# Performance work log

Measured on AMD Instinct MI355X. Metric: run time of the kernel, lower is better.

## Reference

```python
import jax, jax.numpy as jnp
import numpy as np

B, CN, T = 16, 22, 1000
EXP, FCH, SPD, NCLS = 300, 150, 100, 4
KS = (15, 75, 55)
_IU = np.triu_indices(SPD)
_VEC_SCALE = np.where(_IU[0] == _IU[1], 1.0, np.sqrt(2.0)).astype(np.float32)


def _ln(x, g, b, eps=1e-5):
    m = x.mean(-1, keepdims=True)
    v = x.var(-1, keepdims=True)
    return (x - m) / jnp.sqrt(v + eps) * g + b


def _block(x, w1, w2, w3, w4, g1, b1, w5, g2, b2):
    # x: (B, CN, T). Conv2d(1,1,(3,1), same) over electrode axis.
    h = jax.lax.conv_general_dilated(x[:, None], w1.reshape(1, 1, 3, 1), (1, 1),
                                     [(1, 1), (0, 0)],
                                     dimension_numbers=('NCHW', 'OIHW', 'NCHW'))[:, 0]
    # Conv2d(1, 300, (1,1)): pure channel broadcast-expand
    h = h[:, None, :, :] * w2[None, :, None, None]          # (B, EXP, CN, T)
    # Conv2dWithConstraint: depthwise spatial conv (groups=300) with max-norm=1 on each filter
    n = jnp.linalg.norm(w3, axis=1, keepdims=True)
    w3r = w3 * jnp.minimum(1.0, 1.0 / (n + 1e-12))
    h = jnp.einsum('bgct,gc->bgt', h, w3r)                  # height collapses -> (B, EXP, T)
    h = jnp.einsum('og,bgt->bot', w4, h)                    # pointwise -> (B, FCH, T)
    h = _ln(h, g1, b1)
    K = w5.shape[-1]
    # depthwise temporal conv, padding='same' (odd K)
    h = jax.lax.conv_general_dilated(h, w5, (1,), [(K // 2, K // 2)],
                                     dimension_numbers=('NCH', 'OIH', 'NCH'),
                                     feature_group_count=FCH)
    return _ln(h, g2, b2)


def setup_inputs():
    key = jax.random.key(0)
    ks = jax.random.split(key, 64)
    d = {'x': jax.random.normal(ks[0], (B, CN, T), jnp.float32)}
    i = 1
    for bi, K in zip((1, 2, 3), KS):
        d[f'b{bi}_w1'] = jax.random.normal(ks[i], (3,)) / np.sqrt(3); i += 1
        d[f'b{bi}_w2'] = jax.random.normal(ks[i], (EXP,)); i += 1
        d[f'b{bi}_w3'] = jax.random.normal(ks[i], (EXP, CN)) / np.sqrt(CN); i += 1
        d[f'b{bi}_w4'] = jax.random.normal(ks[i], (FCH, EXP)) / np.sqrt(EXP); i += 1
        d[f'b{bi}_g1'] = jnp.ones((T,)); d[f'b{bi}_b1'] = jnp.zeros((T,))
        d[f'b{bi}_w5'] = jax.random.normal(ks[i], (FCH, 1, K)) / np.sqrt(K); i += 1
        d[f'b{bi}_g2'] = jnp.ones((T,)); d[f'b{bi}_b2'] = jnp.zeros((T,))
    d['w_sconv'] = jax.random.normal(ks[i], (SPD, 3 * FCH)) / np.sqrt(3 * FCH); i += 1
    d['w_aff'] = jnp.eye(SPD) + 0.05 * jax.random.normal(ks[i], (SPD, SPD)); i += 1
    d['w_fc'] = jax.random.normal(ks[i], (NCLS, SPD * (SPD + 1) // 2)) / np.sqrt(SPD * (SPD + 1) // 2); i += 1
    d['b_fc'] = jnp.zeros((NCLS,))
    return d


def reference(x,
              b1_w1, b1_w2, b1_w3, b1_w4, b1_g1, b1_b1, b1_w5, b1_g2, b1_b2,
              b2_w1, b2_w2, b2_w3, b2_w4, b2_g1, b2_b1, b2_w5, b2_g2, b2_b2,
              b3_w1, b3_w2, b3_w3, b3_w4, b3_g1, b3_b1, b3_w5, b3_g2, b3_b2,
              w_sconv, w_aff, w_fc, b_fc):
    h1 = _block(x, b1_w1, b1_w2, b1_w3, b1_w4, b1_g1, b1_b1, b1_w5, b1_g2, b1_b2)
    h2 = _block(x, b2_w1, b2_w2, b2_w3, b2_w4, b2_g1, b2_b1, b2_w5, b2_g2, b2_b2)
    h3 = _block(x, b3_w1, b3_w2, b3_w3, b3_w4, b3_g1, b3_b1, b3_w5, b3_g2, b3_b2)
    h = jnp.concatenate([h1, h2, h3], axis=1)               # (B, 450, T)
    h = jnp.einsum('oi,bit->bot', w_sconv, h)               # (B, SPD, T)
    # PCOM: covariance pooling over time -> SPD matrix per sample
    xc = h - h.mean(-1, keepdims=True)
    cov = jnp.einsum('bit,bjt->bij', xc, xc) / (T - 1) + 1e-4 * jnp.eye(SPD)
    # AffineInvariantLayer: learnable congruence transform W P W^T
    P = jnp.einsum('ij,bjk,lk->bil', w_aff, cov, w_aff)
    # LogmLayer: matrix log via batched eigendecomposition
    w, v = jnp.linalg.eigh(P)
    L = jnp.einsum('bik,bk,bjk->bij', v, jnp.log(jnp.clip(w, 1e-6)), v)
    # Vec: upper-triangular half-vectorization (off-diag * sqrt(2)) -> 5050
    flat = L[:, _IU[0], _IU[1]] * _VEC_SCALE
    logits = flat @ w_fc.T + b_fc
    return (logits, flat)
```

## Files before the change

kernel.cpp:

```cpp
#include <hip/hip_runtime.h>

#define B_ 16
#define CN_ 22
#define T_ 1000
#define EXP_ 300
#define FCH_ 150
#define SPD_ 100
#define NSWEEP 8

static constexpr unsigned long long OFF_M2   = 0ull;
static constexpr unsigned long long OFF_HCAT = 65536ull;
static constexpr unsigned long long OFF_XC   = OFF_HCAT + 28800000ull;
static constexpr unsigned long long OFF_COV  = OFF_XC   + 6400000ull;
static constexpr unsigned long long OFF_T1   = OFF_COV  + 640000ull;
static constexpr unsigned long long OFF_P    = OFF_T1   + 640000ull;
static constexpr unsigned long long OFF_G    = OFF_XC;

struct PrepPtrs  { const float* w1[3]; const float* w2[3]; const float* w3[3]; const float* w4[3]; };
struct FrontPtrs { const float* g1[3]; const float* b1[3]; const float* w5[3];
                   const float* g2[3]; const float* b2[3]; int K[3]; };

__device__ __forceinline__ float block_sum(float v, float* sbuf) {
  #pragma unroll
  for (int off = 32; off > 0; off >>= 1) v += __shfl_down(v, off, 64);
  const int wid  = threadIdx.x >> 6;
  const int lane = threadIdx.x & 63;
  const int nw   = blockDim.x >> 6;
  if (lane == 0) sbuf[wid] = v;
  __syncthreads();
  float r = 0.f;
  for (int w = 0; w < nw; ++w) r += sbuf[w];
  __syncthreads();
  return r;
}

__device__ __forceinline__ float dpp_shr1(float old_, float src) {
  return __builtin_bit_cast(float, __builtin_amdgcn_update_dpp(
      __builtin_bit_cast(int, old_), __builtin_bit_cast(int, src),
      0x138, 0xf, 0xf, false));
}
__device__ __forceinline__ float dpp_shl1(float old_, float src) {
  return __builtin_bit_cast(float, __builtin_amdgcn_update_dpp(
      __builtin_bit_cast(int, old_), __builtin_bit_cast(int, src),
      0x130, 0xf, 0xf, false));
}

__global__ __launch_bounds__(256) void k_prep(PrepPtrs pp, float* __restrict__ M2) {
  const int beta = blockIdx.x;
  __shared__ float w3r[EXP_*CN_];
  __shared__ float M[FCH_*CN_];
  const float* w1 = pp.w1[beta];
  const float* w2 = pp.w2[beta];
  const float* w3 = pp.w3[beta];
  const float* w4 = pp.w4[beta];

  for (int g = threadIdx.x; g < EXP_; g += 256) {
    float s = 0.f;
    for (int c = 0; c < CN_; ++c) { float w = w3[g*CN_ + c]; s += w*w; }
    float n = sqrtf(s);
    float scale = fminf(1.f, 1.f/(n + 1e-12f)) * w2[g];
    for (int c = 0; c < CN_; ++c) w3r[g*CN_ + c] = w3[g*CN_ + c] * scale;
  }
  __syncthreads();
  for (int idx = threadIdx.x; idx < FCH_*CN_; idx += 256) {
    int o = idx / CN_, c = idx - o*CN_;
    float acc = 0.f;
    for (int g = 0; g < EXP_; ++g) acc += w4[o*EXP_ + g] * w3r[g*CN_ + c];
    M[idx] = acc;
  }
  __syncthreads();
  const float k0 = w1[0], k1 = w1[1], k2 = w1[2];
  for (int idx = threadIdx.x; idx < FCH_*CN_; idx += 256) {
    int c = idx % CN_;
    float v = k1 * M[idx];
    if (c > 0)       v += k2 * M[idx - 1];
    if (c < CN_ - 1) v += k0 * M[idx + 1];
    M2[beta*FCH_*CN_ + idx] = v;
  }
}

__global__ __launch_bounds__(256) void k_front(const float* __restrict__ x,
                                               const float* __restrict__ M2,
                                               FrontPtrs fp,
                                               float* __restrict__ hcat) {
  const int wg   = blockIdx.x;
  const int beta = wg / (B_*FCH_);
  const int rem  = wg - beta*(B_*FCH_);
  const int b    = rem / FCH_;
  const int o    = rem - b*FCH_;
  const int K    = fp.K[beta];
  const int Kh   = K >> 1;

  __shared__ float m2[CN_];
  __shared__ float hb2[T_];
  __shared__ float w5s[80];
  __shared__ float red[8];

  if (threadIdx.x < CN_) m2[threadIdx.x] = M2[(beta*FCH_ + o)*CN_ + threadIdx.x];
  if (threadIdx.x < K)   w5s[threadIdx.x] = fp.w5[beta][o*K + threadIdx.x];
  __syncthreads();

  const float* xb = x + (size_t)b*CN_*T_;
  float hv[4];
  float psum = 0.f;
  #pragma unroll
  for (int e = 0; e < 4; ++e) {
    int t = threadIdx.x + 256*e;
    float acc = 0.f;
    if (t < T_) {
      #pragma unroll
      for (int c = 0; c < CN_; ++c) acc += m2[c] * xb[c*T_ + t];
    }
    hv[e] = acc; psum += acc;
  }
  float mean = block_sum(psum, red) * (1.f/T_);
  float pv = 0.f;
  #pragma unroll
  for (int e = 0; e < 4; ++e) { int t = threadIdx.x + 256*e; if (t < T_) { float d = hv[e]-mean; pv += d*d; } }
  float var = block_sum(pv, red) * (1.f/T_);
  float inv = rsqrtf(var + 1e-5f);
  const float* g1 = fp.g1[beta]; const float* b1 = fp.b1[beta];
  #pragma unroll
  for (int e = 0; e < 4; ++e) { int t = threadIdx.x + 256*e; if (t < T_) hb2[t] = (hv[e]-mean)*inv*g1[t] + b1[t]; }
  __syncthreads();

  float cv[4];
  float ps2 = 0.f;
  #pragma unroll
  for (int e = 0; e < 4; ++e) {
    int t = threadIdx.x + 256*e;
    float acc = 0.f;
    if (t < T_) {
      int lo = t - Kh;
      for (int k = 0; k < K; ++k) {
        int tt = lo + k;
        float hvv = (tt >= 0 && tt < T_) ? hb2[tt] : 0.f;
        acc += hvv * w5s[k];
      }
    }
    cv[e] = acc; ps2 += acc;
  }
  float mean2 = block_sum(ps2, red) * (1.f/T_);
  float pv2 = 0.f;
  #pragma unroll
  for (int e = 0; e < 4; ++e) { int t = threadIdx.x + 256*e; if (t < T_) { float d = cv[e]-mean2; pv2 += d*d; } }
  float var2 = block_sum(pv2, red) * (1.f/T_);
  float inv2 = rsqrtf(var2 + 1e-5f);
  const float* g2 = fp.g2[beta]; const float* b2 = fp.b2[beta];
  float* hrow = hcat + ((size_t)b*(3*FCH_) + beta*FCH_ + o)*T_;
  #pragma unroll
  for (int e = 0; e < 4; ++e) { int t = threadIdx.x + 256*e; if (t < T_) hrow[t] = (cv[e]-mean2)*inv2*g2[t] + b2[t]; }
}

__global__ __launch_bounds__(256) void k_sconv(const float* __restrict__ hcat,
                                               const float* __restrict__ wsc,
                                               float* __restrict__ xc) {
  const int b  = blockIdx.x / 10;
  const int s0 = (blockIdx.x % 10) * 10;
  __shared__ float ws[10*450];
  __shared__ float red[8];
  for (int idx = threadIdx.x; idx < 4500; idx += 256) {
    int s = idx / 450, i = idx - s*450;
    ws[idx] = wsc[(s0+s)*450 + i];
  }
  __syncthreads();
  float acc[10][4];
  #pragma unroll
  for (int s = 0; s < 10; ++s)
    #pragma unroll
    for (int e = 0; e < 4; ++e) acc[s][e] = 0.f;
  const float* hb = hcat + (size_t)b*450*T_;
  for (int i = 0; i < 450; ++i) {
    float xv[4];
    #pragma unroll
    for (int e = 0; e < 4; ++e) { int t = threadIdx.x + 256*e; xv[e] = (t < T_) ? hb[(size_t)i*T_ + t] : 0.f; }
    #pragma unroll
    for (int s = 0; s < 10; ++s) {
      float w = ws[s*450 + i];
      #pragma unroll
      for (int e = 0; e < 4; ++e) acc[s][e] += w * xv[e];
    }
  }
  for (int s = 0; s < 10; ++s) {
    float mu = block_sum(acc[s][0]+acc[s][1]+acc[s][2]+acc[s][3], red) * (1.f/T_);
    float* xr = xc + ((size_t)b*SPD_ + s0 + s)*T_;
    #pragma unroll
    for (int e = 0; e < 4; ++e) { int t = threadIdx.x + 256*e; if (t < T_) xr[t] = acc[s][e] - mu; }
  }
}

__global__ __launch_bounds__(256) void k_cov(const float* __restrict__ xc, float* __restrict__ cov) {
  const int b  = blockIdx.x / 5;
  const int j0 = (blockIdx.x % 5) * 20;
  __shared__ __align__(16) float xst[SPD_*100];
  const int it = threadIdx.x / 10;
  const int jj = threadIdx.x - it*10;
  const bool act = threadIdx.x < 250;
  double a64[4][2] = {{0.0,0.0},{0.0,0.0},{0.0,0.0},{0.0,0.0}};
  for (int ch = 0; ch < 10; ++ch) {
    __syncthreads();
    const int tc0 = ch*100;
    for (int idx = threadIdx.x; idx < SPD_*100; idx += 256) {
      int row = idx / 100, tt = idx - row*100;
      xst[idx] = xc[((size_t)b*SPD_ + row)*T_ + tc0 + tt];
    }
    __syncthreads();
    if (act) {
      float a32[4][2] = {{0,0},{0,0},{0,0},{0,0}};
      for (int t4 = 0; t4 < 100; t4 += 4) {
        float4 xi[4], xj[2];
        #pragma unroll
        for (int r = 0; r < 4; ++r) xi[r] = *(const float4*)&xst[(it + 25*r)*100 + t4];
        #pragma unroll
        for (int s = 0; s < 2; ++s) xj[s] = *(const float4*)&xst[(j0 + jj + 10*s)*100 + t4];
        #pragma unroll
        for (int r = 0; r < 4; ++r)
          #pragma unroll
          for (int s = 0; s < 2; ++s)
            a32[r][s] += xi[r].x*xj[s].x + xi[r].y*xj[s].y + xi[r].z*xj[s].z + xi[r].w*xj[s].w;
      }
      #pragma unroll
      for (int r = 0; r < 4; ++r)
        #pragma unroll
        for (int s = 0; s < 2; ++s) a64[r][s] += (double)a32[r][s];
    }
  }
  if (act) {
    #pragma unroll
    for (int r = 0; r < 4; ++r) {
      #pragma unroll
      for (int s = 0; s < 2; ++s) {
        int i = it + 25*r, j = j0 + jj + 10*s;
        double v = a64[r][s] * (1.0/999.0);
        if (i == j) v += 1e-4;
        cov[(size_t)b*SPD_*SPD_ + i*SPD_ + j] = (float)v;
      }
    }
  }
}

__global__ __launch_bounds__(256) void k_aff1(const float* __restrict__ cov,
                                              const float* __restrict__ waff,
                                              float* __restrict__ T1) {
  const int b  = blockIdx.x / 5;
  const int j0 = (blockIdx.x % 5) * 20;
  __shared__ float Cs[SPD_*101];
  __shared__ float Ws[20*100];
  for (int idx = threadIdx.x; idx < SPD_*SPD_; idx += 256) {
    int r = idx / 100, c = idx - r*100;
    Cs[r*101 + c] = cov[(size_t)b*SPD_*SPD_ + idx];
  }
  for (int idx = threadIdx.x; idx < 2000; idx += 256) {
    int jl = idx / 100, k = idx - jl*100;
    Ws[idx] = waff[(j0+jl)*100 + k];
  }
  __syncthreads();
  if (threadIdx.x < 250) {
    const int it = threadIdx.x / 10, jj = threadIdx.x % 10;
    double acc[4][2] = {{0.0,0.0},{0.0,0.0},{0.0,0.0},{0.0,0.0}};
    for (int k = 0; k < 100; ++k) {
      double cvv[4], wv[2];
      #pragma unroll
      for (int r = 0; r < 4; ++r) cvv[r] = (double)Cs[(it + 25*r)*101 + k];
      #pragma unroll
      for (int s = 0; s < 2; ++s) wv[s] = (double)Ws[(jj + 10*s)*100 + k];
      #pragma unroll
      for (int r = 0; r < 4; ++r)
        #pragma unroll
        for (int s = 0; s < 2; ++s) acc[r][s] += cvv[r]*wv[s];
    }
    #pragma unroll
    for (int r = 0; r < 4; ++r)
      #pragma unroll
      for (int s = 0; s < 2; ++s)
        T1[(size_t)b*SPD_*SPD_ + (it + 25*r)*100 + (j0 + jj + 10*s)] = (float)acc[r][s];
  }
}

__global__ __launch_bounds__(256) void k_aff2(const float* __restrict__ T1,
                                              const float* __restrict__ waff,
                                              float* __restrict__ P) {
  const int b  = blockIdx.x / 5;
  const int j0 = (blockIdx.x % 5) * 20;
  __shared__ float T1s[100*20];
  for (int idx = threadIdx.x; idx < 2000; idx += 256) {
    int k = idx / 20, jl = idx - k*20;
    T1s[idx] = T1[(size_t)b*SPD_*SPD_ + k*100 + j0 + jl];
  }
  __syncthreads();
  if (threadIdx.x < 250) {
    const int it = threadIdx.x / 10, jj = threadIdx.x % 10;
    double acc[4][2] = {{0.0,0.0},{0.0,0.0},{0.0,0.0},{0.0,0.0}};
    for (int k = 0; k < 100; ++k) {
      double wv[4], tv[2];
      #pragma unroll
      for (int r = 0; r < 4; ++r) wv[r] = (double)waff[(it + 25*r)*100 + k];
      #pragma unroll
      for (int s = 0; s < 2; ++s) tv[s] = (double)T1s[k*20 + jj + 10*s];
      #pragma unroll
      for (int r = 0; r < 4; ++r)
        #pragma unroll
        for (int s = 0; s < 2; ++s) acc[r][s] += wv[r]*tv[s];
    }
    #pragma unroll
    for (int r = 0; r < 4; ++r)
      #pragma unroll
      for (int s = 0; s < 2; ++s)
        P[(size_t)b*SPD_*SPD_ + (it + 25*r)*100 + (j0 + jj + 10*s)] = (float)acc[r][s];
  }
}

__global__ __launch_bounds__(256)
__attribute__((amdgpu_waves_per_eu(1, 1)))
void k_eig(const float* __restrict__ P, float* __restrict__ Gout) {
  __shared__ __align__(16) float gbuf[2][256];
  __shared__ __align__(16) float nbuf[512];
  const int tid = threadIdx.x;
  const int b   = blockIdx.x;
  const int w   = tid >> 6;
  const int j   = tid & 63;
  const bool act = (j < 50);
  const int rb  = 25 * w;

  float A[25], B[25];
  const float* Pb = P + (size_t)b*SPD_*SPD_;
  #pragma unroll
  for (int i = 0; i < 25; ++i) {
    A[i] = act ? Pb[(rb+i)*SPD_ + j]      : 0.f;
    B[i] = act ? Pb[(rb+i)*SPD_ + (99-j)] : 0.f;
  }
  float pA = 0.f, pB = 0.f;
  #pragma unroll
  for (int i = 0; i < 25; ++i) { pA += A[i]*A[i]; pB += B[i]*B[i]; }
  nbuf[j*8 + w*2 + 0] = pA;
  nbuf[j*8 + w*2 + 1] = pB;
  __syncthreads();
  float nA, nB;
  {
    float4 u0 = *(const float4*)&nbuf[j*8];
    float4 u1 = *(const float4*)&nbuf[j*8+4];
    nA = (u0.x + u0.z) + (u1.x + u1.z);
    nB = (u0.y + u0.w) + (u1.y + u1.w);
  }
  float pg = 0.f;
  #pragma unroll
  for (int i = 0; i < 25; ++i) pg += A[i]*B[i];

  int par = 0;
  for (int sweep = 0; sweep < NSWEEP; ++sweep) {
    for (int r = 0; r < 99; ++r) {
      gbuf[par][j*4 + w] = pg;
      __syncthreads();
      float4 gp = *(const float4*)&gbuf[par][j*4];
      float gamma = (gp.x + gp.y) + (gp.z + gp.w);

      float g2 = gamma*gamma;
      float ab = nA*nB;
      float tau = (g2 > 1e-12f*ab) ? ((nB - nA) / (2.f*gamma)) : 1e30f;
      float t  = ((tau >= 0.f) ? 1.f : -1.f) / (fabsf(tau) + sqrtf(1.f + tau*tau));
      float cr = rsqrtf(1.f + t*t);
      float sr = t*cr;
      nA = nA - t*gamma;
      nB = nB + t*gamma;

      {
        float sendN = (j == 0) ? nB : nA;
        float rNA = dpp_shr1(nA, sendN);
        float rNB = dpp_shl1(nB, nB);
        float newB = (j == 49) ? nA : rNB;
        nA = rNA; nB = newB;
      }
      pg = 0.f;
      #pragma unroll
      for (int i = 0; i < 25; ++i) {
        float na = cr*A[i] - sr*B[i];
        float nb = sr*A[i] + cr*B[i];
        float sendA = (j == 0) ? nb : na;
        float rA = dpp_shr1(na, sendA);
        float rB = dpp_shl1(nb, nb);
        A[i] = rA;
        B[i] = (j == 49) ? na : rB;
        pg += A[i]*B[i];
      }
      par ^= 1;
    }
  }

  if (act) {
    float* Gb = Gout + (size_t)b*SPD_*SPD_;
    #pragma unroll
    for (int i = 0; i < 25; ++i) Gb[j*SPD_ + rb + i]        = A[i];
    #pragma unroll
    for (int i = 0; i < 25; ++i) Gb[(50 + j)*SPD_ + rb + i] = B[i];
  }
}

__global__ __launch_bounds__(256) void k_lout(const float* __restrict__ Gin,
                                              const float* __restrict__ wfc,
                                              const float* __restrict__ bfc,
                                              float* __restrict__ out) {
  __shared__ __align__(16) float G[SPD_*SPD_];
  __shared__ float wcs[SPD_];
  __shared__ float red[8];
  const int tid = threadIdx.x;
  const int b   = blockIdx.x;
  for (int idx = tid; idx < SPD_*SPD_; idx += 256)
    G[idx] = Gin[(size_t)b*SPD_*SPD_ + idx];
  __syncthreads();
  if (tid < SPD_) {
    const float* col = &G[tid*SPD_];
    double s = 0.0;
    for (int i = 0; i < SPD_; ++i) { double v = (double)col[i]; s += v*v; }
    double lam = sqrt(s);
    double lc  = (lam < 1e-6) ? 1e-6 : lam;
    wcs[tid] = (float)(log(lc) / ((s > 1e-300) ? s : 1e-300));
  }
  __syncthreads();

  float a0 = 0.f, a1 = 0.f, a2 = 0.f, a3 = 0.f;
  for (int tile = tid; tile < 625; tile += 256) {
    const int ti = (tile / 25) * 4;
    const int tj = (tile % 25) * 4;
    float acc[4][4];
    #pragma unroll
    for (int r = 0; r < 4; ++r)
      #pragma unroll
      for (int s = 0; s < 4; ++s) acc[r][s] = 0.f;
    for (int c = 0; c < SPD_; ++c) {
      const float* col = &G[c*SPD_];
      float4 ga = *(const float4*)&col[ti];
      float4 gb = *(const float4*)&col[tj];
      float wcv = wcs[c];
      float wa[4] = { wcv*ga.x, wcv*ga.y, wcv*ga.z, wcv*ga.w };
      float bv[4] = { gb.x, gb.y, gb.z, gb.w };
      #pragma unroll
      for (int r = 0; r < 4; ++r)
        #pragma unroll
        for (int s = 0; s < 4; ++s) acc[r][s] += wa[r]*bv[s];
    }
    const float RT2 = 1.41421356237309505f;
    #pragma unroll
    for (int r = 0; r < 4; ++r) {
      #pragma unroll
      for (int s = 0; s < 4; ++s) {
        int i = ti + r, jx = tj + s;
        if (i <= jx) {
          int idx = i*SPD_ - (i*(i+1))/2 + jx;
          float val = acc[r][s] * (i == jx ? 1.f : RT2);
          out[64 + b*5050 + idx] = val;
          a0 += val * wfc[idx];
          a1 += val * wfc[5050 + idx];
          a2 += val * wfc[10100 + idx];
          a3 += val * wfc[15150 + idx];
        }
      }
    }
  }
  a0 = block_sum(a0, red);
  a1 = block_sum(a1, red);
  a2 = block_sum(a2, red);
  a3 = block_sum(a3, red);
  if (tid == 0) {
    out[b*4 + 0] = a0 + bfc[0];
    out[b*4 + 1] = a1 + bfc[1];
    out[b*4 + 2] = a2 + bfc[2];
    out[b*4 + 3] = a3 + bfc[3];
  }
}

extern "C" void kernel_launch(void* const* d_in, const int* in_sizes, int n_in,
                              void* d_out, int out_size, void* d_ws, size_t ws_size,
                              hipStream_t stream) {
  (void)in_sizes; (void)n_in; (void)out_size; (void)ws_size;
  const float* x = (const float*)d_in[0];
  const float* bw[3][9];
  for (int i = 0; i < 3; ++i)
    for (int jx = 0; jx < 9; ++jx)
      bw[i][jx] = (const float*)d_in[1 + i*9 + jx];
  const float* w_sconv = (const float*)d_in[28];
  const float* w_aff   = (const float*)d_in[29];
  const float* w_fc    = (const float*)d_in[30];
  const float* b_fc    = (const float*)d_in[31];

  char* ws = (char*)d_ws;
  float*  M2   = (float*)(ws + OFF_M2);
  float*  hcat = (float*)(ws + OFF_HCAT);
  float*  xc   = (float*)(ws + OFF_XC);
  float*  cov  = (float*)(ws + OFF_COV);
  float*  T1   = (float*)(ws + OFF_T1);
  float*  P    = (float*)(ws + OFF_P);
  float*  G    = (float*)(ws + OFF_G);
  float*  out  = (float*)d_out;

  PrepPtrs pp; FrontPtrs fp;
  for (int i = 0; i < 3; ++i) {
    pp.w1[i] = bw[i][0]; pp.w2[i] = bw[i][1]; pp.w3[i] = bw[i][2]; pp.w4[i] = bw[i][3];
    fp.g1[i] = bw[i][4]; fp.b1[i] = bw[i][5]; fp.w5[i] = bw[i][6];
    fp.g2[i] = bw[i][7]; fp.b2[i] = bw[i][8];
  }
  fp.K[0] = 15; fp.K[1] = 75; fp.K[2] = 55;

  hipLaunchKernelGGL(k_prep,  dim3(3),            dim3(256), 0, stream, pp, M2);
  hipLaunchKernelGGL(k_front, dim3(3*B_*FCH_),    dim3(256), 0, stream, x, M2, fp, hcat);
  hipLaunchKernelGGL(k_sconv, dim3(B_*10),        dim3(256), 0, stream, hcat, w_sconv, xc);
  hipLaunchKernelGGL(k_cov,   dim3(B_*5),         dim3(256), 0, stream, xc, cov);
  hipLaunchKernelGGL(k_aff1,  dim3(B_*5),         dim3(256), 0, stream, cov, w_aff, T1);
  hipLaunchKernelGGL(k_aff2,  dim3(B_*5),         dim3(256), 0, stream, T1, w_aff, P);
  hipLaunchKernelGGL(k_eig,   dim3(B_),           dim3(256), 0, stream, P, G);
  hipLaunchKernelGGL(k_lout,  dim3(B_),           dim3(256), 0, stream, G, w_fc, b_fc, out);
}
```

Measured before the change: 1.260 ms.

## Fuse affine congruence kernels and pack Jacobi rotations into float2 vectors

Merges the two affine-transform kernels into one: the intermediate cov·Wᵀ tile stays in shared memory, which removes a global round trip and a launch. The Jacobi eigen-solver now holds its column pairs in 2-wide float vectors so the rotation arithmetic can map to packed FP32 instructions, with one scalar element left over from the 25-row split. The DPP lane shifts are still done per component, and register use and the summation order change slightly.

```diff
diff --git a/kernel.cpp b/kernel.cpp
--- a/kernel.cpp
+++ b/kernel.cpp
@@ -8,12 +8,13 @@
 #define SPD_ 100
 #define NSWEEP 8
 
+typedef float v2f __attribute__((ext_vector_type(2)));
+
 static constexpr unsigned long long OFF_M2   = 0ull;
 static constexpr unsigned long long OFF_HCAT = 65536ull;
 static constexpr unsigned long long OFF_XC   = OFF_HCAT + 28800000ull;
 static constexpr unsigned long long OFF_COV  = OFF_XC   + 6400000ull;
-static constexpr unsigned long long OFF_T1   = OFF_COV  + 640000ull;
-static constexpr unsigned long long OFF_P    = OFF_T1   + 640000ull;
+static constexpr unsigned long long OFF_P    = OFF_COV  + 640000ull;
 static constexpr unsigned long long OFF_G    = OFF_XC;
 
 struct PrepPtrs  { const float* w1[3]; const float* w2[3]; const float* w3[3]; const float* w4[3]; };
@@ -239,13 +240,14 @@
   }
 }
 
-__global__ __launch_bounds__(256) void k_aff1(const float* __restrict__ cov,
-                                              const float* __restrict__ waff,
-                                              float* __restrict__ T1) {
+__global__ __launch_bounds__(256) void k_aff(const float* __restrict__ cov,
+                                             const float* __restrict__ waff,
+                                             float* __restrict__ P) {
   const int b  = blockIdx.x / 5;
   const int j0 = (blockIdx.x % 5) * 20;
   __shared__ float Cs[SPD_*101];
   __shared__ float Ws[20*100];
+  __shared__ float T1s[100*20];
   for (int idx = threadIdx.x; idx < SPD_*SPD_; idx += 256) {
     int r = idx / 100, c = idx - r*100;
     Cs[r*101 + c] = cov[(size_t)b*SPD_*SPD_ + idx];
@@ -255,8 +257,9 @@
     Ws[idx] = waff[(j0+jl)*100 + k];
   }
   __syncthreads();
-  if (threadIdx.x < 250) {
-    const int it = threadIdx.x / 10, jj = threadIdx.x % 10;
+  const int it = threadIdx.x / 10, jj = threadIdx.x % 10;
+  const bool act = threadIdx.x < 250;
+  if (act) {
     double acc[4][2] = {{0.0,0.0},{0.0,0.0},{0.0,0.0},{0.0,0.0}};
     for (int k = 0; k < 100; ++k) {
       double cvv[4], wv[2];
@@ -273,23 +276,10 @@
     for (int r = 0; r < 4; ++r)
       #pragma unroll
       for (int s = 0; s < 2; ++s)
-        T1[(size_t)b*SPD_*SPD_ + (it + 25*r)*100 + (j0 + jj + 10*s)] = (float)acc[r][s];
-  }
-}
-
-__global__ __launch_bounds__(256) void k_aff2(const float* __restrict__ T1,
-                                              const float* __restrict__ waff,
-                                              float* __restrict__ P) {
-  const int b  = blockIdx.x / 5;
-  const int j0 = (blockIdx.x % 5) * 20;
-  __shared__ float T1s[100*20];
-  for (int idx = threadIdx.x; idx < 2000; idx += 256) {
-    int k = idx / 20, jl = idx - k*20;
-    T1s[idx] = T1[(size_t)b*SPD_*SPD_ + k*100 + j0 + jl];
-  }
-  __syncthreads();
-  if (threadIdx.x < 250) {
-    const int it = threadIdx.x / 10, jj = threadIdx.x % 10;
+        T1s[(it + 25*r)*20 + (jj + 10*s)] = (float)acc[r][s];
+  }
+  __syncthreads();
+  if (act) {
     double acc[4][2] = {{0.0,0.0},{0.0,0.0},{0.0,0.0},{0.0,0.0}};
     for (int k = 0; k < 100; ++k) {
       double wv[4], tv[2];
@@ -322,18 +312,26 @@
   const bool act = (j < 50);
   const int rb  = 25 * w;
 
-  float A[25], B[25];
+  v2f A2[12], B2[12];
+  float As, Bs;
   const float* Pb = P + (size_t)b*SPD_*SPD_;
   #pragma unroll
-  for (int i = 0; i < 25; ++i) {
-    A[i] = act ? Pb[(rb+i)*SPD_ + j]      : 0.f;
-    B[i] = act ? Pb[(rb+i)*SPD_ + (99-j)] : 0.f;
-  }
-  float pA = 0.f, pB = 0.f;
-  #pragma unroll
-  for (int i = 0; i < 25; ++i) { pA += A[i]*A[i]; pB += B[i]*B[i]; }
-  nbuf[j*8 + w*2 + 0] = pA;
-  nbuf[j*8 + w*2 + 1] = pB;
+  for (int i = 0; i < 12; ++i) {
+    A2[i].x = act ? Pb[(rb+2*i  )*SPD_ + j]      : 0.f;
+    A2[i].y = act ? Pb[(rb+2*i+1)*SPD_ + j]      : 0.f;
+    B2[i].x = act ? Pb[(rb+2*i  )*SPD_ + (99-j)] : 0.f;
+    B2[i].y = act ? Pb[(rb+2*i+1)*SPD_ + (99-j)] : 0.f;
+  }
+  As = act ? Pb[(rb+24)*SPD_ + j]      : 0.f;
+  Bs = act ? Pb[(rb+24)*SPD_ + (99-j)] : 0.f;
+
+  {
+    v2f pA2 = {0.f, 0.f}, pB2 = {0.f, 0.f};
+    #pragma unroll
+    for (int i = 0; i < 12; ++i) { pA2 += A2[i]*A2[i]; pB2 += B2[i]*B2[i]; }
+    nbuf[j*8 + w*2 + 0] = pA2.x + pA2.y + As*As;
+    nbuf[j*8 + w*2 + 1] = pB2.x + pB2.y + Bs*Bs;
+  }
   __syncthreads();
   float nA, nB;
   {
@@ -342,9 +340,13 @@
     nA = (u0.x + u0.z) + (u1.x + u1.z);
     nB = (u0.y + u0.w) + (u1.y + u1.w);
   }
-  float pg = 0.f;
-  #pragma unroll
-  for (int i = 0; i < 25; ++i) pg += A[i]*B[i];
+  float pg;
+  {
+    v2f pg2 = {0.f, 0.f};
+    #pragma unroll
+    for (int i = 0; i < 12; ++i) pg2 += A2[i]*B2[i];
+    pg = pg2.x + pg2.y + As*Bs;
+  }
 
   int par = 0;
   for (int sweep = 0; sweep < NSWEEP; ++sweep) {
@@ -354,9 +356,9 @@
       float4 gp = *(const float4*)&gbuf[par][j*4];
       float gamma = (gp.x + gp.y) + (gp.z + gp.w);
 
-      float g2 = gamma*gamma;
+      float g2v = gamma*gamma;
       float ab = nA*nB;
-      float tau = (g2 > 1e-12f*ab) ? ((nB - nA) / (2.f*gamma)) : 1e30f;
+      float tau = (g2v > 1e-12f*ab) ? ((nB - nA) / (2.f*gamma)) : 1e30f;
       float t  = ((tau >= 0.f) ? 1.f : -1.f) / (fabsf(tau) + sqrtf(1.f + tau*tau));
       float cr = rsqrtf(1.f + t*t);
       float sr = t*cr;
@@ -370,18 +372,35 @@
         float newB = (j == 49) ? nA : rNB;
         nA = rNA; nB = newB;
       }
-      pg = 0.f;
-      #pragma unroll
-      for (int i = 0; i < 25; ++i) {
-        float na = cr*A[i] - sr*B[i];
-        float nb = sr*A[i] + cr*B[i];
-        float sendA = (j == 0) ? nb : na;
-        float rA = dpp_shr1(na, sendA);
+      const v2f cr2 = {cr, cr};
+      const v2f sr2 = {sr, sr};
+      v2f pg2 = {0.f, 0.f};
+      #pragma unroll
+      for (int i = 0; i < 12; ++i) {
+        v2f na = cr2*A2[i] - sr2*B2[i];
+        v2f nb = sr2*A2[i] + cr2*B2[i];
+        float sx = (j == 0) ? nb.x : na.x;
+        float sy = (j == 0) ? nb.y : na.y;
+        v2f rA, rB;
+        rA.x = dpp_shr1(na.x, sx);
+        rA.y = dpp_shr1(na.y, sy);
+        rB.x = dpp_shl1(nb.x, nb.x);
+        rB.y = dpp_shl1(nb.y, nb.y);
+        A2[i] = rA;
+        B2[i].x = (j == 49) ? na.x : rB.x;
+        B2[i].y = (j == 49) ? na.y : rB.y;
+        pg2 += A2[i]*B2[i];
+      }
+      {
+        float na = cr*As - sr*Bs;
+        float nb = sr*As + cr*Bs;
+        float sA = (j == 0) ? nb : na;
+        float rA = dpp_shr1(na, sA);
         float rB = dpp_shl1(nb, nb);
-        A[i] = rA;
-        B[i] = (j == 49) ? na : rB;
-        pg += A[i]*B[i];
-      }
+        As = rA;
+        Bs = (j == 49) ? na : rB;
+      }
+      pg = pg2.x + pg2.y + As*Bs;
       par ^= 1;
     }
   }
@@ -389,9 +408,14 @@
   if (act) {
     float* Gb = Gout + (size_t)b*SPD_*SPD_;
     #pragma unroll
-    for (int i = 0; i < 25; ++i) Gb[j*SPD_ + rb + i]        = A[i];
-    #pragma unroll
-    for (int i = 0; i < 25; ++i) Gb[(50 + j)*SPD_ + rb + i] = B[i];
+    for (int i = 0; i < 12; ++i) {
+      Gb[j*SPD_ + rb + 2*i]   = A2[i].x;
+      Gb[j*SPD_ + rb + 2*i+1] = A2[i].y;
+      Gb[(50 + j)*SPD_ + rb + 2*i]   = B2[i].x;
+      Gb[(50 + j)*SPD_ + rb + 2*i+1] = B2[i].y;
+    }
+    Gb[j*SPD_ + rb + 24]        = As;
+    Gb[(50 + j)*SPD_ + rb + 24] = Bs;
   }
 }
 
@@ -487,7 +511,6 @@
   float*  hcat = (float*)(ws + OFF_HCAT);
   float*  xc   = (float*)(ws + OFF_XC);
   float*  cov  = (float*)(ws + OFF_COV);
-  float*  T1   = (float*)(ws + OFF_T1);
   float*  P    = (float*)(ws + OFF_P);
   float*  G    = (float*)(ws + OFF_G);
   float*  out  = (float*)d_out;
@@ -504,8 +527,7 @@
   hipLaunchKernelGGL(k_front, dim3(3*B_*FCH_),    dim3(256), 0, stream, x, M2, fp, hcat);
   hipLaunchKernelGGL(k_sconv, dim3(B_*10),        dim3(256), 0, stream, hcat, w_sconv, xc);
   hipLaunchKernelGGL(k_cov,   dim3(B_*5),         dim3(256), 0, stream, xc, cov);
-  hipLaunchKernelGGL(k_aff1,  dim3(B_*5),         dim3(256), 0, stream, cov, w_aff, T1);
-  hipLaunchKernelGGL(k_aff2,  dim3(B_*5),         dim3(256), 0, stream, T1, w_aff, P);
+  hipLaunchKernelGGL(k_aff,   dim3(B_*5),         dim3(256), 0, stream, cov, w_aff, P);
   hipLaunchKernelGGL(k_eig,   dim3(B_),           dim3(256), 0, stream, P, G);
   hipLaunchKernelGGL(k_lout,  dim3(B_),           dim3(256), 0, stream, G, w_fc, b_fc, out);
 }
```

New measurement: 1.102 ms. 12.5% less time.
